# Optimization experiments

Hardware: AMD Instinct MI355X
Metric: run time of the kernel (lower is better)

Reference implementation:

```python
import jax, jax.numpy as jnp
import numpy as np

B, T, D, H = 32, 512, 512, 1024


def setup_inputs() -> dict:
    key = jax.random.key(0)
    k1, k2, k3 = jax.random.split(key, 3)
    X = jax.random.normal(k1, (B, T, D), dtype=jnp.float32)
    # TF GRUCell variables: gates/kernel [D+H, 2H], gates/bias [2H] (init 1.0),
    # candidate/kernel [D+H, H], candidate/bias [H] (init 0.0). Use small random
    # values for a non-degenerate numerical baseline.
    gate_kernel = jax.random.normal(k2, (D + H, 2 * H), dtype=jnp.float32) * 0.02
    gate_bias = jnp.ones((2 * H,), dtype=jnp.float32)
    cand_kernel = jax.random.normal(k3, (D + H, H), dtype=jnp.float32) * 0.02
    cand_bias = jnp.zeros((H,), dtype=jnp.float32)
    return {"X": X, "gate_kernel": gate_kernel, "gate_bias": gate_bias,
            "cand_kernel": cand_kernel, "cand_bias": cand_bias}


def reference(X, gate_kernel, gate_bias, cand_kernel, cand_bias):
    """Static unidirectional GRU (TF GRUCell math), activation=tanh.
    Returns stacked per-step hidden states [B, T, H]; final state is out[:, -1]."""
    h0 = jnp.zeros((X.shape[0], cand_kernel.shape[1]), dtype=X.dtype)

    def step(h, x_t):
        # gates: r (reset), u (update) = sigmoid([x, h] @ Wg + bg)
        gates = jax.nn.sigmoid(jnp.concatenate([x_t, h], axis=-1) @ gate_kernel + gate_bias)
        r, u = jnp.split(gates, 2, axis=-1)
        # candidate: tanh([x, r*h] @ Wc + bc)
        c = jnp.tanh(jnp.concatenate([x_t, r * h], axis=-1) @ cand_kernel + cand_bias)
        h_new = u * h + (1.0 - u) * c
        return h_new, h_new

    _, hs = jax.lax.scan(step, h0, jnp.swapaxes(X, 0, 1))  # hs: [T, B, H]
    return jnp.swapaxes(hs, 0, 1)  # [B, T, H]
```

## Files before the change

kernel.cpp:

```cpp
#include <hip/hip_runtime.h>
#include <hip/hip_bf16.h>

typedef short s8v __attribute__((ext_vector_type(8)));
typedef float f4v __attribute__((ext_vector_type(4)));
typedef unsigned int u4v __attribute__((ext_vector_type(4)));
typedef unsigned int u2v __attribute__((ext_vector_type(2)));

#define NBLK 64
#define TPB 512

constexpr int BB = 32, TT = 512, DD = 512, HH = 1024;
constexpr int KK = DD + HH;
constexpr int PK = KK + 8;
constexpr int PK8 = PK / 8;
constexpr int K8 = KK / 8;
constexpr size_t BBHH = (size_t)BB * HH;

constexpr size_t OFF_WGT = 0;
constexpr size_t SZ_WGT  = (size_t)2 * HH * KK * 2;
constexpr size_t OFF_WCT = OFF_WGT + SZ_WGT;
constexpr size_t SZ_WCT  = (size_t)HH * KK * 2;
constexpr size_t OFF_XBF = OFF_WCT + SZ_WCT;
constexpr size_t SZ_XBF  = (size_t)BB * TT * DD * 2;
constexpr size_t OFF_HPB = OFF_XBF + SZ_XBF;
constexpr size_t SZ_PUB1 = BBHH * 2;
constexpr size_t SZ_PUBT = SZ_PUB1 * TT;
constexpr size_t SZ_FLG  = (size_t)2 * NBLK * 2 * 16 * 4;
constexpr size_t OFF_RPB_D = OFF_HPB + SZ_PUBT;
constexpr size_t OFF_FLG_D = OFF_RPB_D + SZ_PUBT;
constexpr size_t NEED_D    = OFF_FLG_D + SZ_FLG;
constexpr size_t OFF_RPB_S = OFF_HPB + SZ_PUB1;
constexpr size_t OFF_FLG_S = OFF_RPB_S + SZ_PUB1;
constexpr size_t NEED_S    = OFF_FLG_S + SZ_FLG;

__global__ void wtr_kernel(const float* __restrict__ in, unsigned short* __restrict__ out, int N) {
    __shared__ float tl[32][33];
    int tx = threadIdx.x & 31, ty = threadIdx.x >> 5;
    int n0 = blockIdx.x * 32, k0 = blockIdx.y * 32;
#pragma unroll
    for (int r = ty; r < 32; r += 8) tl[r][tx] = in[(size_t)(k0 + r) * N + n0 + tx];
    __syncthreads();
#pragma unroll
    for (int r = ty; r < 32; r += 8) {
        __hip_bfloat16 h = __float2bfloat16(tl[tx][r]);
        out[(size_t)(n0 + r) * KK + k0 + tx] = *reinterpret_cast<unsigned short*>(&h);
    }
}

__global__ void xconv_kernel(const float* __restrict__ X, unsigned short* __restrict__ Xbf) {
    size_t i = ((size_t)blockIdx.x * 256 + threadIdx.x) * 4;
    float4 v = *reinterpret_cast<const float4*>(X + i);
    __hip_bfloat16 h0 = __float2bfloat16(v.x), h1 = __float2bfloat16(v.y);
    __hip_bfloat16 h2 = __float2bfloat16(v.z), h3 = __float2bfloat16(v.w);
    ushort4 o;
    o.x = *(unsigned short*)&h0; o.y = *(unsigned short*)&h1;
    o.z = *(unsigned short*)&h2; o.w = *(unsigned short*)&h3;
    *reinterpret_cast<ushort4*>(Xbf + i) = o;
}

__device__ __forceinline__ u4v cload16(const void* p) {
    u4v r; asm volatile("global_load_dwordx4 %0, %1, off sc0 sc1" : "=v"(r) : "v"(p) : "memory"); return r;
}
__device__ __forceinline__ void cstore8(void* p, u2v v) {
    asm volatile("global_store_dwordx2 %0, %1, off sc0 sc1" :: "v"(p), "v"(v) : "memory");
}
#define B16(x) __builtin_bit_cast(s8v, (x))
#define WAIT_VM(n) do { asm volatile("s_waitcnt vmcnt(" #n ")" ::: "memory"); \
                        __builtin_amdgcn_sched_barrier(0); } while (0)

__device__ __forceinline__ void poll16(const int* f, int blk0, int rtw, int gen, int lane) {
    if (lane < 16) {
        const int* fp = f + ((size_t)(blk0 + lane) * 2 + rtw) * 16;
        while (__hip_atomic_load(fp, __ATOMIC_RELAXED, __HIP_MEMORY_SCOPE_AGENT) < gen)
            __builtin_amdgcn_s_sleep(1);
    }
    asm volatile("" ::: "memory");
}

#define MFMA(A, B, C) __builtin_amdgcn_mfma_f32_16x16x32_bf16((A), (B), (C), 0, 0, 0)

template<bool DEEP>
__global__ __launch_bounds__(TPB, 1) void gru_kernel(
    const unsigned short* __restrict__ Xbf,
    const unsigned short* __restrict__ WgT,
    const unsigned short* __restrict__ WcT,
    const float* __restrict__ bg,
    const float* __restrict__ bc,
    float* __restrict__ out,
    unsigned short* __restrict__ hpub,
    unsigned short* __restrict__ rpub,
    int* __restrict__ gflagA,
    int* __restrict__ gflagB)
{
    __shared__ unsigned short sWg[32 * PK];
    __shared__ unsigned short sWc[16 * PK];
    __shared__ float sP[3][2][2][16][16];
    __shared__ unsigned short sStage[2][16][16];

    const int b    = blockIdx.x;
    const int tid  = threadIdx.x;
    const int wid  = tid >> 6;
    const int lane = tid & 63;
    const int l15  = lane & 15;
    const int lq   = lane >> 4;
    const int ks   = wid >> 1;
    const int rt   = wid & 1;
    const int roff = rt * 16;
    const int arow = roff + l15;
    const int bcol0= b * 16;

    {
        s8v* dst = (s8v*)sWg;
        for (int idx = tid; idx < 32 * K8; idx += TPB) {
            int c = idx / K8, k8 = idx % K8;
            int gc = (c < 16) ? (bcol0 + c) : (HH + bcol0 + (c - 16));
            dst[c * PK8 + k8] = ((const s8v*)(WgT + (size_t)gc * KK))[k8];
        }
        s8v* dst2 = (s8v*)sWc;
        for (int idx = tid; idx < 16 * K8; idx += TPB) {
            int c = idx / K8, k8 = idx % K8;
            dst2[c * PK8 + k8] = ((const s8v*)(WcT + (size_t)(bcol0 + c) * KK))[k8];
        }
    }

    const float bgr  = bg[bcol0 + l15];
    const float bgu  = bg[HH + bcol0 + l15];
    const float bcv  = bc[bcol0 + l15];
    const int   ccol = bcol0 + l15;

    const s8v* sWg8 = (const s8v*)sWg;
    const s8v* sWc8 = (const s8v*)sWc;
    const s8v* bwr = sWg8 + l15 * PK8 + lq;
    const s8v* bwu = sWg8 + (16 + l15) * PK8 + lq;
    const s8v* bwc = sWc8 + l15 * PK8 + lq;
    const s8v* bwrx = bwr + 16 * ks;
    const s8v* bwux = bwu + 16 * ks;
    const s8v* bwrh = bwr + 64 + 32 * ks;
    const s8v* bwuh = bwu + 64 + 32 * ks;
    const s8v* bwcx = bwc + 16 * ks;
    const s8v* bwch = bwc + 64 + 32 * ks;

    float hprev[4] = {0.f, 0.f, 0.f, 0.f};
    float ureg[4]  = {0.f, 0.f, 0.f, 0.f};

    __syncthreads();

#pragma unroll 1
    for (int t = 0; t < TT; ++t) {
        const s8v* xk = (const s8v*)(Xbf + (size_t)arow * (TT * DD) + (size_t)t * DD) + lq + 16 * ks;
        s8v x0 = xk[0], x1 = xk[4], x2 = xk[8], x3 = xk[12];

        f4v ar0 = {0,0,0,0}, ar1 = {0,0,0,0}, au0 = {0,0,0,0}, au1 = {0,0,0,0};
        if (t > 0) {
            poll16(gflagB, ks * 16, rt, t, lane);
            const unsigned short* hp = hpub + (DEEP ? (size_t)(t - 1) * BBHH : 0)
                                     + (size_t)arow * HH + ks * 256 + lq * 8;
            u4v hb[8];
            if (DEEP) {
#pragma unroll
                for (int j = 0; j < 8; ++j) hb[j] = *reinterpret_cast<const u4v*>(hp + (size_t)j * 32);
                ar0 = MFMA(x0, bwrx[0],  ar0); au0 = MFMA(x0, bwux[0],  au0);
                ar1 = MFMA(x1, bwrx[4],  ar1); au1 = MFMA(x1, bwux[4],  au1);
                ar0 = MFMA(x2, bwrx[8],  ar0); au0 = MFMA(x2, bwux[8],  au0);
                ar1 = MFMA(x3, bwrx[12], ar1); au1 = MFMA(x3, bwux[12], au1);
            } else {
#pragma unroll
                for (int j = 0; j < 8; ++j) hb[j] = cload16(hp + (size_t)j * 32);
                ar0 = MFMA(x0, bwrx[0],  ar0); au0 = MFMA(x0, bwux[0],  au0);
                ar1 = MFMA(x1, bwrx[4],  ar1); au1 = MFMA(x1, bwux[4],  au1);
                ar0 = MFMA(x2, bwrx[8],  ar0); au0 = MFMA(x2, bwux[8],  au0);
                ar1 = MFMA(x3, bwrx[12], ar1); au1 = MFMA(x3, bwux[12], au1);
                WAIT_VM(0);
            }
            ar0 = MFMA(B16(hb[0]), bwrh[0],  ar0); au0 = MFMA(B16(hb[0]), bwuh[0],  au0);
            ar1 = MFMA(B16(hb[1]), bwrh[4],  ar1); au1 = MFMA(B16(hb[1]), bwuh[4],  au1);
            ar0 = MFMA(B16(hb[2]), bwrh[8],  ar0); au0 = MFMA(B16(hb[2]), bwuh[8],  au0);
            ar1 = MFMA(B16(hb[3]), bwrh[12], ar1); au1 = MFMA(B16(hb[3]), bwuh[12], au1);
            ar0 = MFMA(B16(hb[4]), bwrh[16], ar0); au0 = MFMA(B16(hb[4]), bwuh[16], au0);
            ar1 = MFMA(B16(hb[5]), bwrh[20], ar1); au1 = MFMA(B16(hb[5]), bwuh[20], au1);
            ar0 = MFMA(B16(hb[6]), bwrh[24], ar0); au0 = MFMA(B16(hb[6]), bwuh[24], au0);
            ar1 = MFMA(B16(hb[7]), bwrh[28], ar1); au1 = MFMA(B16(hb[7]), bwuh[28], au1);
        } else {
            ar0 = MFMA(x0, bwrx[0],  ar0); au0 = MFMA(x0, bwux[0],  au0);
            ar1 = MFMA(x1, bwrx[4],  ar1); au1 = MFMA(x1, bwux[4],  au1);
            ar0 = MFMA(x2, bwrx[8],  ar0); au0 = MFMA(x2, bwux[8],  au0);
            ar1 = MFMA(x3, bwrx[12], ar1); au1 = MFMA(x3, bwux[12], au1);
        }

        f4v pr = ar0 + ar1, pu = au0 + au1;
        if (ks > 0) {
#pragma unroll
            for (int i = 0; i < 4; ++i) {
                sP[ks - 1][rt][0][lq * 4 + i][l15] = pr[i];
                sP[ks - 1][rt][1][lq * 4 + i][l15] = pu[i];
            }
        }
        __syncthreads();
        float zr[4], zu[4];
        if (ks == 0) {
#pragma unroll
            for (int i = 0; i < 4; ++i) {
                int rr = lq * 4 + i;
                zr[i] = pr[i] + sP[0][rt][0][rr][l15] + sP[1][rt][0][rr][l15]
                              + sP[2][rt][0][rr][l15] + bgr;
                zu[i] = pu[i] + sP[0][rt][1][rr][l15] + sP[1][rt][1][rr][l15]
                              + sP[2][rt][1][rr][l15] + bgu;
            }
        }
        __syncthreads();
        if (ks == 0) {
#pragma unroll
            for (int i = 0; i < 4; ++i) {
                float r = 1.f / (1.f + __expf(-zr[i]));
                ureg[i] = 1.f / (1.f + __expf(-zu[i]));
                __hip_bfloat16 hb16 = __float2bfloat16(r * hprev[i]);
                sStage[rt][lq * 4 + i][l15] = *(unsigned short*)&hb16;
            }
            if (t > 0) {
                int prow = lane >> 2, pc4 = (lane & 3) * 4;
                u2v v = *reinterpret_cast<const u2v*>(&sStage[rt][prow][pc4]);
                cstore8(rpub + (DEEP ? (size_t)t * BBHH : 0)
                             + (size_t)(roff + prow) * HH + bcol0 + pc4, v);
                asm volatile("s_waitcnt vmcnt(0)" ::: "memory");
                if (lane == 0)
                    __hip_atomic_store(&gflagA[(b * 2 + rt) * 16], t,
                                       __ATOMIC_RELAXED, __HIP_MEMORY_SCOPE_AGENT);
            }
        }

        f4v c0 = {0,0,0,0}, c1 = {0,0,0,0};
        if (t > 0) {
            poll16(gflagA, ks * 16, rt, t, lane);
            const unsigned short* rp = rpub + (DEEP ? (size_t)t * BBHH : 0)
                                     + (size_t)arow * HH + ks * 256 + lq * 8;
            u4v rb[8];
            if (DEEP) {
#pragma unroll
                for (int j = 0; j < 8; ++j) rb[j] = *reinterpret_cast<const u4v*>(rp + (size_t)j * 32);
                c0 = MFMA(x0, bwcx[0],  c0); c1 = MFMA(x1, bwcx[4],  c1);
                c0 = MFMA(x2, bwcx[8],  c0); c1 = MFMA(x3, bwcx[12], c1);
            } else {
#pragma unroll
                for (int j = 0; j < 8; ++j) rb[j] = cload16(rp + (size_t)j * 32);
                c0 = MFMA(x0, bwcx[0],  c0); c1 = MFMA(x1, bwcx[4],  c1);
                c0 = MFMA(x2, bwcx[8],  c0); c1 = MFMA(x3, bwcx[12], c1);
                WAIT_VM(0);
            }
            c0 = MFMA(B16(rb[0]), bwch[0],  c0); c1 = MFMA(B16(rb[1]), bwch[4],  c1);
            c0 = MFMA(B16(rb[2]), bwch[8],  c0); c1 = MFMA(B16(rb[3]), bwch[12], c1);
            c0 = MFMA(B16(rb[4]), bwch[16], c0); c1 = MFMA(B16(rb[5]), bwch[20], c1);
            c0 = MFMA(B16(rb[6]), bwch[24], c0); c1 = MFMA(B16(rb[7]), bwch[28], c1);
        } else {
            c0 = MFMA(x0, bwcx[0],  c0); c1 = MFMA(x1, bwcx[4],  c1);
            c0 = MFMA(x2, bwcx[8],  c0); c1 = MFMA(x3, bwcx[12], c1);
        }

        f4v pc = c0 + c1;
        if (ks > 0) {
#pragma unroll
            for (int i = 0; i < 4; ++i) sP[ks - 1][rt][0][lq * 4 + i][l15] = pc[i];
        }
        __syncthreads();
        float zc[4];
        if (ks == 0) {
#pragma unroll
            for (int i = 0; i < 4; ++i) {
                int rr = lq * 4 + i;
                zc[i] = pc[i] + sP[0][rt][0][rr][l15] + sP[1][rt][0][rr][l15]
                              + sP[2][rt][0][rr][l15] + bcv;
            }
        }
        __syncthreads();
        if (ks == 0) {
#pragma unroll
            for (int i = 0; i < 4; ++i) {
                float e = __expf(2.f * zc[i]);
                float cv = 1.f - 2.f / (e + 1.f);
                float hn = ureg[i] * hprev[i] + (1.f - ureg[i]) * cv;
                hprev[i] = hn;
                __hip_bfloat16 hb16 = __float2bfloat16(hn);
                sStage[rt][lq * 4 + i][l15] = *(unsigned short*)&hb16;
            }
            int prow = lane >> 2, pc4 = (lane & 3) * 4;
            u2v v = *reinterpret_cast<const u2v*>(&sStage[rt][prow][pc4]);
            cstore8(hpub + (DEEP ? (size_t)t * BBHH : 0)
                         + (size_t)(roff + prow) * HH + bcol0 + pc4, v);
            asm volatile("s_waitcnt vmcnt(0)" ::: "memory");
            if (lane == 0)
                __hip_atomic_store(&gflagB[(b * 2 + rt) * 16], t + 1,
                                   __ATOMIC_RELAXED, __HIP_MEMORY_SCOPE_AGENT);
#pragma unroll
            for (int i = 0; i < 4; ++i) {
                int row = roff + lq * 4 + i;
                out[(size_t)row * (TT * HH) + (size_t)t * HH + ccol] = hprev[i];
            }
        }
    }
}

extern "C" void kernel_launch(void* const* d_in, const int* in_sizes, int n_in,
                              void* d_out, int out_size, void* d_ws, size_t ws_size,
                              hipStream_t stream) {
    const float* X  = (const float*)d_in[0];
    const float* gk = (const float*)d_in[1];
    const float* gb = (const float*)d_in[2];
    const float* ck = (const float*)d_in[3];
    const float* cb = (const float*)d_in[4];
    float* out = (float*)d_out;
    char* ws = (char*)d_ws;
    if (ws_size < NEED_S) return;

    const bool deep = (ws_size >= NEED_D);

    unsigned short* WgT  = (unsigned short*)(ws + OFF_WGT);
    unsigned short* WcT  = (unsigned short*)(ws + OFF_WCT);
    unsigned short* Xbf  = (unsigned short*)(ws + OFF_XBF);
    unsigned short* hpub = (unsigned short*)(ws + OFF_HPB);
    unsigned short* rpub = (unsigned short*)(ws + (deep ? OFF_RPB_D : OFF_RPB_S));
    int*            gflagA = (int*)(ws + (deep ? OFF_FLG_D : OFF_FLG_S));
    int*            gflagB = gflagA + NBLK * 2 * 16;

    hipMemsetAsync(gflagA, 0, SZ_FLG, stream);

    dim3 tb(256);
    wtr_kernel<<<dim3(2 * HH / 32, KK / 32), tb, 0, stream>>>(gk, WgT, 2 * HH);
    wtr_kernel<<<dim3(HH / 32, KK / 32), tb, 0, stream>>>(ck, WcT, HH);
    xconv_kernel<<<(BB * TT * DD) / (256 * 4), tb, 0, stream>>>(X, Xbf);

    if (deep)
        gru_kernel<true><<<NBLK, dim3(TPB), 0, stream>>>(Xbf, WgT, WcT, gb, cb, out,
                                                         hpub, rpub, gflagA, gflagB);
    else
        gru_kernel<false><<<NBLK, dim3(TPB), 0, stream>>>(Xbf, WgT, WcT, gb, cb, out,
                                                          hpub, rpub, gflagA, gflagB);
}
```

Measured before the change: 4.025 ms.

## Replace flag polling with sentinel-filled per-step buffers for cross-block sync

Drops the per-step atomic flag publish/poll handshake between blocks. Instead, the per-timestep h and r publication buffers are prefilled with 0xFF and consumers spin-reload any 16-byte chunk still holding an all-ones word. This removes the store-wait-then-flag round trip from the recurrent critical path. In exchange it requires a full-size per-timestep workspace and a large memset before launch. It also relies on bf16 data never producing a 0xFFFFFFFF word (a NaN pattern) and on the 16-byte stores becoming visible atomically.

```diff
diff --git a/kernel.cpp b/kernel.cpp
--- a/kernel.cpp
+++ b/kernel.cpp
@@ -23,15 +23,9 @@
 constexpr size_t OFF_XBF = OFF_WCT + SZ_WCT;
 constexpr size_t SZ_XBF  = (size_t)BB * TT * DD * 2;
 constexpr size_t OFF_HPB = OFF_XBF + SZ_XBF;
-constexpr size_t SZ_PUB1 = BBHH * 2;
-constexpr size_t SZ_PUBT = SZ_PUB1 * TT;
-constexpr size_t SZ_FLG  = (size_t)2 * NBLK * 2 * 16 * 4;
-constexpr size_t OFF_RPB_D = OFF_HPB + SZ_PUBT;
-constexpr size_t OFF_FLG_D = OFF_RPB_D + SZ_PUBT;
-constexpr size_t NEED_D    = OFF_FLG_D + SZ_FLG;
-constexpr size_t OFF_RPB_S = OFF_HPB + SZ_PUB1;
-constexpr size_t OFF_FLG_S = OFF_RPB_S + SZ_PUB1;
-constexpr size_t NEED_S    = OFF_FLG_S + SZ_FLG;
+constexpr size_t SZ_PUBT = BBHH * 2 * TT;
+constexpr size_t OFF_RPB = OFF_HPB + SZ_PUBT;
+constexpr size_t NEED    = OFF_RPB + SZ_PUBT;
 
 __global__ void wtr_kernel(const float* __restrict__ in, unsigned short* __restrict__ out, int N) {
     __shared__ float tl[32][33];
@@ -68,18 +62,13 @@
 #define WAIT_VM(n) do { asm volatile("s_waitcnt vmcnt(" #n ")" ::: "memory"); \
                         __builtin_amdgcn_sched_barrier(0); } while (0)
 
-__device__ __forceinline__ void poll16(const int* f, int blk0, int rtw, int gen, int lane) {
-    if (lane < 16) {
-        const int* fp = f + ((size_t)(blk0 + lane) * 2 + rtw) * 16;
-        while (__hip_atomic_load(fp, __ATOMIC_RELAXED, __HIP_MEMORY_SCOPE_AGENT) < gen)
-            __builtin_amdgcn_s_sleep(1);
-    }
-    asm volatile("" ::: "memory");
+__device__ __forceinline__ int dirty16(u4v v) {
+    return (v[0] == 0xFFFFFFFFu) | (v[1] == 0xFFFFFFFFu) |
+           (v[2] == 0xFFFFFFFFu) | (v[3] == 0xFFFFFFFFu);
 }
 
 #define MFMA(A, B, C) __builtin_amdgcn_mfma_f32_16x16x32_bf16((A), (B), (C), 0, 0, 0)
 
-template<bool DEEP>
 __global__ __launch_bounds__(TPB, 1) void gru_kernel(
     const unsigned short* __restrict__ Xbf,
     const unsigned short* __restrict__ WgT,
@@ -88,9 +77,7 @@
     const float* __restrict__ bc,
     float* __restrict__ out,
     unsigned short* __restrict__ hpub,
-    unsigned short* __restrict__ rpub,
-    int* __restrict__ gflagA,
-    int* __restrict__ gflagB)
+    unsigned short* __restrict__ rpub)
 {
     __shared__ unsigned short sWg[32 * PK];
     __shared__ unsigned short sWc[16 * PK];
@@ -152,25 +139,22 @@
 
         f4v ar0 = {0,0,0,0}, ar1 = {0,0,0,0}, au0 = {0,0,0,0}, au1 = {0,0,0,0};
         if (t > 0) {
-            poll16(gflagB, ks * 16, rt, t, lane);
-            const unsigned short* hp = hpub + (DEEP ? (size_t)(t - 1) * BBHH : 0)
+            const unsigned short* hp = hpub + (size_t)(t - 1) * BBHH
                                      + (size_t)arow * HH + ks * 256 + lq * 8;
             u4v hb[8];
-            if (DEEP) {
-#pragma unroll
-                for (int j = 0; j < 8; ++j) hb[j] = *reinterpret_cast<const u4v*>(hp + (size_t)j * 32);
-                ar0 = MFMA(x0, bwrx[0],  ar0); au0 = MFMA(x0, bwux[0],  au0);
-                ar1 = MFMA(x1, bwrx[4],  ar1); au1 = MFMA(x1, bwux[4],  au1);
-                ar0 = MFMA(x2, bwrx[8],  ar0); au0 = MFMA(x2, bwux[8],  au0);
-                ar1 = MFMA(x3, bwrx[12], ar1); au1 = MFMA(x3, bwux[12], au1);
-            } else {
-#pragma unroll
-                for (int j = 0; j < 8; ++j) hb[j] = cload16(hp + (size_t)j * 32);
-                ar0 = MFMA(x0, bwrx[0],  ar0); au0 = MFMA(x0, bwux[0],  au0);
-                ar1 = MFMA(x1, bwrx[4],  ar1); au1 = MFMA(x1, bwux[4],  au1);
-                ar0 = MFMA(x2, bwrx[8],  ar0); au0 = MFMA(x2, bwux[8],  au0);
-                ar1 = MFMA(x3, bwrx[12], ar1); au1 = MFMA(x3, bwux[12], au1);
-                WAIT_VM(0);
+#pragma unroll
+            for (int j = 0; j < 8; ++j) hb[j] = cload16(hp + (size_t)j * 32);
+            ar0 = MFMA(x0, bwrx[0],  ar0); au0 = MFMA(x0, bwux[0],  au0);
+            ar1 = MFMA(x1, bwrx[4],  ar1); au1 = MFMA(x1, bwux[4],  au1);
+            ar0 = MFMA(x2, bwrx[8],  ar0); au0 = MFMA(x2, bwux[8],  au0);
+            ar1 = MFMA(x3, bwrx[12], ar1); au1 = MFMA(x3, bwux[12], au1);
+            WAIT_VM(0);
+#pragma unroll
+            for (int j = 0; j < 8; ++j) {
+                while (__builtin_expect(dirty16(hb[j]), 0)) {
+                    hb[j] = cload16(hp + (size_t)j * 32);
+                    asm volatile("s_waitcnt vmcnt(0)" ::: "memory");
+                }
             }
             ar0 = MFMA(B16(hb[0]), bwrh[0],  ar0); au0 = MFMA(B16(hb[0]), bwuh[0],  au0);
             ar1 = MFMA(B16(hb[1]), bwrh[4],  ar1); au1 = MFMA(B16(hb[1]), bwuh[4],  au1);
@@ -219,32 +203,26 @@
             if (t > 0) {
                 int prow = lane >> 2, pc4 = (lane & 3) * 4;
                 u2v v = *reinterpret_cast<const u2v*>(&sStage[rt][prow][pc4]);
-                cstore8(rpub + (DEEP ? (size_t)t * BBHH : 0)
-                             + (size_t)(roff + prow) * HH + bcol0 + pc4, v);
-                asm volatile("s_waitcnt vmcnt(0)" ::: "memory");
-                if (lane == 0)
-                    __hip_atomic_store(&gflagA[(b * 2 + rt) * 16], t,
-                                       __ATOMIC_RELAXED, __HIP_MEMORY_SCOPE_AGENT);
+                cstore8(rpub + (size_t)t * BBHH + (size_t)(roff + prow) * HH + bcol0 + pc4, v);
             }
         }
 
         f4v c0 = {0,0,0,0}, c1 = {0,0,0,0};
         if (t > 0) {
-            poll16(gflagA, ks * 16, rt, t, lane);
-            const unsigned short* rp = rpub + (DEEP ? (size_t)t * BBHH : 0)
+            const unsigned short* rp = rpub + (size_t)t * BBHH
                                      + (size_t)arow * HH + ks * 256 + lq * 8;
             u4v rb[8];
-            if (DEEP) {
-#pragma unroll
-                for (int j = 0; j < 8; ++j) rb[j] = *reinterpret_cast<const u4v*>(rp + (size_t)j * 32);
-                c0 = MFMA(x0, bwcx[0],  c0); c1 = MFMA(x1, bwcx[4],  c1);
-                c0 = MFMA(x2, bwcx[8],  c0); c1 = MFMA(x3, bwcx[12], c1);
-            } else {
-#pragma unroll
-                for (int j = 0; j < 8; ++j) rb[j] = cload16(rp + (size_t)j * 32);
-                c0 = MFMA(x0, bwcx[0],  c0); c1 = MFMA(x1, bwcx[4],  c1);
-                c0 = MFMA(x2, bwcx[8],  c0); c1 = MFMA(x3, bwcx[12], c1);
-                WAIT_VM(0);
+#pragma unroll
+            for (int j = 0; j < 8; ++j) rb[j] = cload16(rp + (size_t)j * 32);
+            c0 = MFMA(x0, bwcx[0],  c0); c1 = MFMA(x1, bwcx[4],  c1);
+            c0 = MFMA(x2, bwcx[8],  c0); c1 = MFMA(x3, bwcx[12], c1);
+            WAIT_VM(0);
+#pragma unroll
+            for (int j = 0; j < 8; ++j) {
+                while (__builtin_expect(dirty16(rb[j]), 0)) {
+                    rb[j] = cload16(rp + (size_t)j * 32);
+                    asm volatile("s_waitcnt vmcnt(0)" ::: "memory");
+                }
             }
             c0 = MFMA(B16(rb[0]), bwch[0],  c0); c1 = MFMA(B16(rb[1]), bwch[4],  c1);
             c0 = MFMA(B16(rb[2]), bwch[8],  c0); c1 = MFMA(B16(rb[3]), bwch[12], c1);
@@ -283,12 +261,7 @@
             }
             int prow = lane >> 2, pc4 = (lane & 3) * 4;
             u2v v = *reinterpret_cast<const u2v*>(&sStage[rt][prow][pc4]);
-            cstore8(hpub + (DEEP ? (size_t)t * BBHH : 0)
-                         + (size_t)(roff + prow) * HH + bcol0 + pc4, v);
-            asm volatile("s_waitcnt vmcnt(0)" ::: "memory");
-            if (lane == 0)
-                __hip_atomic_store(&gflagB[(b * 2 + rt) * 16], t + 1,
-                                   __ATOMIC_RELAXED, __HIP_MEMORY_SCOPE_AGENT);
+            cstore8(hpub + (size_t)t * BBHH + (size_t)(roff + prow) * HH + bcol0 + pc4, v);
 #pragma unroll
             for (int i = 0; i < 4; ++i) {
                 int row = roff + lq * 4 + i;
@@ -308,29 +281,21 @@
     const float* cb = (const float*)d_in[4];
     float* out = (float*)d_out;
     char* ws = (char*)d_ws;
-    if (ws_size < NEED_S) return;
-
-    const bool deep = (ws_size >= NEED_D);
+    if (ws_size < NEED) return;
 
     unsigned short* WgT  = (unsigned short*)(ws + OFF_WGT);
     unsigned short* WcT  = (unsigned short*)(ws + OFF_WCT);
     unsigned short* Xbf  = (unsigned short*)(ws + OFF_XBF);
     unsigned short* hpub = (unsigned short*)(ws + OFF_HPB);
-    unsigned short* rpub = (unsigned short*)(ws + (deep ? OFF_RPB_D : OFF_RPB_S));
-    int*            gflagA = (int*)(ws + (deep ? OFF_FLG_D : OFF_FLG_S));
-    int*            gflagB = gflagA + NBLK * 2 * 16;
-
-    hipMemsetAsync(gflagA, 0, SZ_FLG, stream);
+    unsigned short* rpub = (unsigned short*)(ws + OFF_RPB);
+
+    hipMemsetAsync(hpub, 0xFF, 2 * SZ_PUBT, stream);
 
     dim3 tb(256);
     wtr_kernel<<<dim3(2 * HH / 32, KK / 32), tb, 0, stream>>>(gk, WgT, 2 * HH);
     wtr_kernel<<<dim3(HH / 32, KK / 32), tb, 0, stream>>>(ck, WcT, HH);
     xconv_kernel<<<(BB * TT * DD) / (256 * 4), tb, 0, stream>>>(X, Xbf);
 
-    if (deep)
-        gru_kernel<true><<<NBLK, dim3(TPB), 0, stream>>>(Xbf, WgT, WcT, gb, cb, out,
-                                                         hpub, rpub, gflagA, gflagB);
-    else
-        gru_kernel<false><<<NBLK, dim3(TPB), 0, stream>>>(Xbf, WgT, WcT, gb, cb, out,
-                                                          hpub, rpub, gflagA, gflagB);
-}
+    gru_kernel<<<NBLK, dim3(TPB), 0, stream>>>(Xbf, WgT, WcT, gb, cb, out,
+                                               hpub, rpub);
+}
```

Measured after the change: 5.151 ms. 28.0% more time.
